# Kernel optimization log

Measured on AMD Instinct MI355X. Metric: run time of the kernel, lower is better.

Reference implementation:

```python
import jax, jax.numpy as jnp
import numpy as np

B, D, H, L = 65536, 512, 1024, 64
LOG2PI = float(np.log(2.0 * np.pi))


def setup_inputs() -> dict:
    key = jax.random.key(0)
    ks = jax.random.split(key, 16)
    s = jnp.float32(0.02)

    def w(k, shape):
        return jax.random.normal(k, shape, dtype=jnp.float32) * s

    return {
        "x": jax.random.normal(ks[0], (B, D), dtype=jnp.float32),
        "eps": jax.random.normal(ks[1], (B, L), dtype=jnp.float32),
        # encoder params (Linear stored as [in, out] for x @ W + b)
        "W_enc_h": w(ks[2], (D, H)), "b_enc_h": jnp.zeros((H,), jnp.float32),
        "W_enc_mu": w(ks[3], (H, L)), "b_enc_mu": jnp.zeros((L,), jnp.float32),
        "W_enc_lv": w(ks[4], (H, L)), "b_enc_lv": jnp.zeros((L,), jnp.float32),
        # decoder params
        "W_dec_h": w(ks[5], (L, H)), "b_dec_h": jnp.zeros((H,), jnp.float32),
        "W_dec_mu": w(ks[6], (H, D)), "b_dec_mu": jnp.zeros((D,), jnp.float32),
        "W_dec_lv": w(ks[7], (H, D)), "b_dec_lv": jnp.zeros((D,), jnp.float32),
    }


def reference(x, eps, W_enc_h, b_enc_h, W_enc_mu, b_enc_mu, W_enc_lv, b_enc_lv,
              W_dec_h, b_dec_h, W_dec_mu, b_dec_mu, W_dec_lv, b_dec_lv):
    beta = jnp.float32(1.0)
    # encoder
    h = jnp.tanh(x @ W_enc_h + b_enc_h)                      # [B, H]
    mu_z = h @ W_enc_mu + b_enc_mu                           # [B, L]
    lv_z = h @ W_enc_lv + b_enc_lv                           # [B, L]
    # reparameterised sample
    z = mu_z + jnp.exp(0.5 * lv_z) * eps                     # [B, L]
    # decoder
    hd = jnp.tanh(z @ W_dec_h + b_dec_h)                     # [B, H]
    mu_x = jax.nn.softmax(hd @ W_dec_mu + b_dec_mu, axis=-1) # [B, D]
    lv_x = hd @ W_dec_lv + b_dec_lv                          # [B, D]
    # KL(q(z|x) || N(0, I))
    kl = -0.5 * jnp.sum(1.0 + lv_z - mu_z ** 2 - jnp.exp(lv_z), axis=-1)  # [B]
    # diagonal Gaussian log-likelihood (closed form of MultivariateNormal
    # with diag_embed(exp(ln_var)) covariance)
    ln_pxz = -0.5 * jnp.sum(lv_x + (x - mu_x) ** 2 * jnp.exp(-lv_x) + LOG2PI, axis=-1)  # [B]
    return jnp.mean(ln_pxz - beta * kl)
```

## Files before the change

kernel.cpp:

```cpp
#include <hip/hip_runtime.h>

typedef unsigned char u8;
typedef unsigned short u16;
typedef unsigned int u32;
typedef long i64;
typedef __attribute__((ext_vector_type(2))) long long2v;
typedef __attribute__((ext_vector_type(4))) float floatx4;

#define LOG2PI_F 1.8378770664093453f

__device__ __forceinline__ u16 f2bf(float f) {
  union { float f; u32 i; } c; c.f = f;
  u32 i = c.i;
  u32 r = (i + 0x7fffu + ((i >> 16) & 1u)) >> 16;
  return (u16)r;
}
__device__ __forceinline__ float bf2f(u16 u) {
  union { u32 i; float f; } c; c.i = ((u32)u) << 16; return c.f;
}
__device__ __forceinline__ u8 f2fp8(float f) {
  int p = __builtin_amdgcn_cvt_pk_fp8_f32(f, f, 0, false);
  return (u8)(p & 0xff);
}
__device__ __forceinline__ u32 pk4fp8(float a, float b, float c, float d) {
  int lo = __builtin_amdgcn_cvt_pk_fp8_f32(a, b, 0, false);
  int v  = __builtin_amdgcn_cvt_pk_fp8_f32(c, d, lo, true);
  return (u32)v;
}
__device__ __forceinline__ void llds16(const void* g, void* l) {
  __builtin_amdgcn_global_load_lds(
      (const __attribute__((address_space(1))) u32*)g,
      (__attribute__((address_space(3))) u32*)l, 16, 0, 0);
}
__device__ __forceinline__ u32 permk(u32 k) {
  u32 g = k & ~63u, o = (k >> 3) & 7u, r = k & 7u;
  u32 po = ((o & 3u) << 1) | (o >> 2);
  return g | (po << 3) | r;
}

#define INV_4096  2.44140625e-4f
#define INV_16384 6.103515625e-5f

__global__ void pack_xb(const float* __restrict__ in, u32* __restrict__ out, int n4) {
  int i = blockIdx.x * 256 + threadIdx.x;
  if (i >= n4) return;
  const float4 v = ((const float4*)in)[i];
  int row = i >> 7;
  int k = (i & 127) << 2;
  int kp = permk(k);
  out[(row << 7) + (kp >> 2)] = pk4fp8(v.x * 16.f, v.y * 16.f, v.z * 16.f, v.w * 16.f);
}

__global__ void pack_wt(const float* __restrict__ W, u8* __restrict__ Wt, int K, int N) {
  int idx = blockIdx.x * 256 + threadIdx.x;
  if (idx >= K * N) return;
  int k = idx / N, n = idx - k * N;
  Wt[(size_t)n * K + permk(k)] = f2fp8(W[idx] * 256.f);
}

__global__ void pack_wt2(const float* __restrict__ W1, const float* __restrict__ W2,
                         u8* __restrict__ Wt, int K, int N1, int N2) {
  int idx = blockIdx.x * 256 + threadIdx.x;
  if (idx >= (N1 + N2) * K) return;
  int n = idx / K, k = idx - n * K;
  float v = (n < N1) ? W1[(size_t)k * N1 + n] : W2[(size_t)k * N2 + (n - N1)];
  Wt[(size_t)n * K + permk(k)] = f2fp8(v * 256.f);
}

__global__ void catf(const float* __restrict__ a, const float* __restrict__ b,
                     float* __restrict__ o, int n1, int n2) {
  int i = blockIdx.x * 256 + threadIdx.x;
  if (i < n1) o[i] = a[i];
  else if (i < n1 + n2) o[i] = b[i - n1];
}

template <int EPI>
__global__ __launch_bounds__(256) void gemm_bt(
    const u8* __restrict__ A, const u8* __restrict__ Bt,
    const float* __restrict__ bias, void* __restrict__ Cv,
    float inv, float outs, int M, int N, int K) {
  __shared__ __align__(16) u8 As[128 * 64];
  __shared__ __align__(16) u8 Bs[128 * 64];
  const int t = threadIdx.x;
  const int wave = t >> 6, lane = t & 63;
  const int quad = lane >> 4, l16 = lane & 15;
  const int bm = blockIdx.y * 128, bn = blockIdx.x * 128;
  const int wm = (wave >> 1) * 64, wn = (wave & 1) * 64;

  floatx4 acc[4][4];
#pragma unroll
  for (int i = 0; i < 4; ++i)
#pragma unroll
    for (int j = 0; j < 4; ++j) acc[i][j] = (floatx4){0.f, 0.f, 0.f, 0.f};

  for (int kt = 0; kt < K; kt += 64) {
#pragma unroll
    for (int i = 0; i < 2; ++i) {
      int c = i * 256 + t;
      int r = c >> 2, kcS = c & 3;
      int kc = kcS ^ ((r >> 1) & 3);
      llds16(A + (size_t)(bm + r) * K + kt + kc * 16, &As[c * 16]);
      llds16(Bt + (size_t)(bn + r) * K + kt + kc * 16, &Bs[c * 16]);
    }
    __builtin_amdgcn_s_waitcnt(0);
    __syncthreads();

    long2v a2[4], b2[4];
#pragma unroll
    for (int mi = 0; mi < 4; ++mi) {
      int m = wm + mi * 16 + l16;
      a2[mi] = *(const long2v*)&As[(4 * m + (quad ^ ((m >> 1) & 3))) * 16];
    }
#pragma unroll
    for (int ni = 0; ni < 4; ++ni) {
      int n = wn + ni * 16 + l16;
      b2[ni] = *(const long2v*)&Bs[(4 * n + (quad ^ ((n >> 1) & 3))) * 16];
    }
#pragma unroll
    for (int h = 0; h < 2; ++h)
#pragma unroll
      for (int mi = 0; mi < 4; ++mi)
#pragma unroll
        for (int ni = 0; ni < 4; ++ni)
          acc[mi][ni] = __builtin_amdgcn_mfma_f32_16x16x32_fp8_fp8(
              a2[mi][h], b2[ni][h], acc[mi][ni], 0, 0, 0);
    __syncthreads();
  }

#pragma unroll
  for (int ni = 0; ni < 4; ++ni) {
    int col = bn + wn + ni * 16 + l16;
    float bv = bias[col];
#pragma unroll
    for (int mi = 0; mi < 4; ++mi) {
#pragma unroll
      for (int r = 0; r < 4; ++r) {
        int row = bm + wm + mi * 16 + quad * 4 + r;
        float v = acc[mi][ni][r] * inv + bv;
        if (EPI == 0) {
          ((u8*)Cv)[(size_t)row * N + permk(col)] = f2fp8(tanhf(v) * outs);
        } else {
          ((u16*)Cv)[(size_t)row * N + col] = f2bf(v);
        }
      }
    }
  }
}

__global__ __launch_bounds__(256) void gemm_z(
    const u8* __restrict__ A, const u8* __restrict__ Bt,
    const float* __restrict__ bias, const float* __restrict__ eps,
    u8* __restrict__ z, float* __restrict__ accp, int M, int K) {
  __shared__ __align__(16) u8 As[128 * 64];
  __shared__ __align__(16) u8 Bs[128 * 64];
  __shared__ float sexp[128 * 64];
  const int t = threadIdx.x;
  const int wave = t >> 6, lane = t & 63;
  const int quad = lane >> 4, l16 = lane & 15;
  const int bm = blockIdx.y * 128;
  const int wm = (wave >> 1) * 64, wn = (wave & 1) * 64;

  floatx4 acc[4][4];
#pragma unroll
  for (int i = 0; i < 4; ++i)
#pragma unroll
    for (int j = 0; j < 4; ++j) acc[i][j] = (floatx4){0.f, 0.f, 0.f, 0.f};

  for (int kt = 0; kt < K; kt += 64) {
#pragma unroll
    for (int i = 0; i < 2; ++i) {
      int c = i * 256 + t;
      int r = c >> 2, kcS = c & 3;
      int kc = kcS ^ ((r >> 1) & 3);
      llds16(A + (size_t)(bm + r) * K + kt + kc * 16, &As[c * 16]);
      llds16(Bt + (size_t)r * K + kt + kc * 16, &Bs[c * 16]);
    }
    __builtin_amdgcn_s_waitcnt(0);
    __syncthreads();

    long2v a2[4], b2[4];
#pragma unroll
    for (int mi = 0; mi < 4; ++mi) {
      int m = wm + mi * 16 + l16;
      a2[mi] = *(const long2v*)&As[(4 * m + (quad ^ ((m >> 1) & 3))) * 16];
    }
#pragma unroll
    for (int ni = 0; ni < 4; ++ni) {
      int n = wn + ni * 16 + l16;
      b2[ni] = *(const long2v*)&Bs[(4 * n + (quad ^ ((n >> 1) & 3))) * 16];
    }
#pragma unroll
    for (int h = 0; h < 2; ++h)
#pragma unroll
      for (int mi = 0; mi < 4; ++mi)
#pragma unroll
        for (int ni = 0; ni < 4; ++ni)
          acc[mi][ni] = __builtin_amdgcn_mfma_f32_16x16x32_fp8_fp8(
              a2[mi][h], b2[ni][h], acc[mi][ni], 0, 0, 0);
    __syncthreads();
  }

  const bool is_lv = (wave & 1);
  float kl = 0.f;
#pragma unroll
  for (int ni = 0; ni < 4; ++ni) {
    int col = wn + ni * 16 + l16;
    float bv = bias[col];
#pragma unroll
    for (int mi = 0; mi < 4; ++mi) {
#pragma unroll
      for (int r = 0; r < 4; ++r) {
        int row = wm + mi * 16 + quad * 4 + r;
        float v = acc[mi][ni][r] * INV_16384 + bv;
        if (is_lv) {
          kl += 1.0f + v - __expf(v);
          sexp[row * 64 + (col - 64)] = __expf(0.5f * v);
        } else {
          kl -= v * v;
        }
      }
    }
  }
  __syncthreads();
  if (!is_lv) {
#pragma unroll
    for (int ni = 0; ni < 4; ++ni) {
      int col = wn + ni * 16 + l16;
      float bv = bias[col];
#pragma unroll
      for (int mi = 0; mi < 4; ++mi) {
#pragma unroll
        for (int r = 0; r < 4; ++r) {
          int row = wm + mi * 16 + quad * 4 + r;
          float mu = acc[mi][ni][r] * INV_16384 + bv;
          size_t grow = (size_t)(bm + row);
          float ep = eps[grow * 64 + col];
          z[grow * 64 + permk(col)] = f2fp8((mu + sexp[row * 64 + col] * ep) * 16.f);
        }
      }
    }
  }
  kl *= 0.5f;
  for (int off = 32; off > 0; off >>= 1) kl += __shfl_xor(kl, off, 64);
  __shared__ float s4[4];
  if (lane == 0) s4[wave] = kl;
  __syncthreads();
  if (t == 0) atomicAdd(accp, s4[0] + s4[1] + s4[2] + s4[3]);
}

__global__ __launch_bounds__(256) void lik_kernel(
    const u16* __restrict__ loglv, const float* __restrict__ x,
    float* __restrict__ acc) {
  typedef __attribute__((ext_vector_type(8))) short short8;
  const int wave = threadIdx.x >> 6, lane = threadIdx.x & 63;
  float wacc = 0.f;
  for (int rr = 0; rr < 8; ++rr) {
    int row = blockIdx.x * 32 + wave * 8 + rr;
    const u16* Lr = loglv + (size_t)row * 1024;
    short8 lg8 = ((const short8*)Lr)[lane];
    float lg[8];
#pragma unroll
    for (int j = 0; j < 8; ++j) lg[j] = bf2f((u16)lg8[j]);
    float mx = lg[0];
#pragma unroll
    for (int j = 1; j < 8; ++j) mx = fmaxf(mx, lg[j]);
    for (int off = 32; off > 0; off >>= 1) mx = fmaxf(mx, __shfl_xor(mx, off, 64));
    float e[8], s = 0.f;
#pragma unroll
    for (int j = 0; j < 8; ++j) { e[j] = __expf(lg[j] - mx); s += e[j]; }
    for (int off = 32; off > 0; off >>= 1) s += __shfl_xor(s, off, 64);
    float inv_s = 1.0f / s;
    short8 lv8 = ((const short8*)Lr)[64 + lane];
    const float* xr = x + (size_t)row * 512 + lane * 8;
    float4 x0 = *(const float4*)xr, x1 = *(const float4*)(xr + 4);
    float xs[8] = {x0.x, x0.y, x0.z, x0.w, x1.x, x1.y, x1.z, x1.w};
    float T = 0.f;
#pragma unroll
    for (int j = 0; j < 8; ++j) {
      float lv = bf2f((u16)lv8[j]);
      float d = xs[j] - e[j] * inv_s;
      T += lv + d * d * __expf(-lv) + LOG2PI_F;
    }
    for (int off = 32; off > 0; off >>= 1) T += __shfl_xor(T, off, 64);
    if (lane == 0) wacc += -0.5f * T;
  }
  __shared__ float s4[4];
  if (lane == 0) s4[wave] = wacc;
  __syncthreads();
  if (threadIdx.x == 0) atomicAdd(acc, s4[0] + s4[1] + s4[2] + s4[3]);
}

__global__ void fin_kernel(const float* __restrict__ acc, float* __restrict__ out) {
  out[0] = acc[0] * (1.0f / 65536.0f);
}

extern "C" void kernel_launch(void* const* d_in, const int* in_sizes, int n_in,
                              void* d_out, int out_size, void* d_ws, size_t ws_size,
                              hipStream_t stream) {
  const int B = 65536, D = 512, H = 1024, L = 64;
  const float* x       = (const float*)d_in[0];
  const float* eps     = (const float*)d_in[1];
  const float* W_enc_h = (const float*)d_in[2];
  const float* b_enc_h = (const float*)d_in[3];
  const float* W_enc_mu= (const float*)d_in[4];
  const float* b_enc_mu= (const float*)d_in[5];
  const float* W_enc_lv= (const float*)d_in[6];
  const float* b_enc_lv= (const float*)d_in[7];
  const float* W_dec_h = (const float*)d_in[8];
  const float* b_dec_h = (const float*)d_in[9];
  const float* W_dec_mu= (const float*)d_in[10];
  const float* b_dec_mu= (const float*)d_in[11];
  const float* W_dec_lv= (const float*)d_in[12];
  const float* b_dec_lv= (const float*)d_in[13];

  char* ws = (char*)d_ws;
  u8*   Wt_eh  = (u8*)(ws + 0);
  u8*   Wt_z   = (u8*)(ws + 524288);
  u8*   Wt_dh  = (u8*)(ws + 655360);
  u8*   Wt_dx  = (u8*)(ws + 720896);
  float* bh    = (float*)(ws + 2097152);
  float* bz    = (float*)(ws + 2101248);
  float* bdh   = (float*)(ws + 2105344);
  float* bdx   = (float*)(ws + 2109440);
  float* acc   = (float*)(ws + 2113536);
  u8*   hbuf   = (u8*)(ws + 4194304);
  u8*   xb     = (u8*)(ws + 71303168);
  u8*   zbuf   = (u8*)(ws + 104857600);
  u16*  loglv  = (u16*)(ws + 109051904);

  hipMemsetAsync(acc, 0, 256, stream);

  pack_xb<<<(B * D / 4 + 255) / 256, 256, 0, stream>>>(x, (u32*)xb, B * D / 4);
  pack_wt<<<(D * H + 255) / 256, 256, 0, stream>>>(W_enc_h, Wt_eh, D, H);
  pack_wt2<<<(H * 2 * L + 255) / 256, 256, 0, stream>>>(W_enc_mu, W_enc_lv, Wt_z, H, L, L);
  pack_wt<<<(L * H + 255) / 256, 256, 0, stream>>>(W_dec_h, Wt_dh, L, H);
  pack_wt2<<<(H * 2 * D + 255) / 256, 256, 0, stream>>>(W_dec_mu, W_dec_lv, Wt_dx, H, D, D);
  catf<<<(H + 255) / 256, 256, 0, stream>>>(b_enc_h, b_enc_h, bh, H, 0);
  catf<<<(2 * L + 255) / 256, 256, 0, stream>>>(b_enc_mu, b_enc_lv, bz, L, L);
  catf<<<(H + 255) / 256, 256, 0, stream>>>(b_dec_h, b_dec_h, bdh, H, 0);
  catf<<<(2 * D + 255) / 256, 256, 0, stream>>>(b_dec_mu, b_dec_lv, bdx, D, D);

  gemm_bt<0><<<dim3(H / 128, B / 128), 256, 0, stream>>>(
      xb, Wt_eh, bh, hbuf, INV_4096, 64.f, B, H, D);
  gemm_z<<<dim3(1, B / 128), 256, 0, stream>>>(hbuf, Wt_z, bz, eps, zbuf, acc, B, H);
  gemm_bt<0><<<dim3(H / 128, B / 128), 256, 0, stream>>>(
      zbuf, Wt_dh, bdh, hbuf, INV_4096, 64.f, B, H, L);
  gemm_bt<2><<<dim3(1024 / 128, B / 128), 256, 0, stream>>>(
      hbuf, Wt_dx, bdx, loglv, INV_16384, 0.f, B, 1024, H);
  lik_kernel<<<B / 32, 256, 0, stream>>>(loglv, x, acc);
  fin_kernel<<<1, 1, 0, stream>>>(acc, (float*)d_out);
}
```

Measured before the change: 618.7 us.

## Add 256x256-tile FP8 GEMM with 4-stage LDS pipeline for large GEMMs

```diff
diff --git a/kernel.cpp b/kernel.cpp
--- a/kernel.cpp
+++ b/kernel.cpp
@@ -133,6 +133,108 @@
     float bv = bias[col];
 #pragma unroll
     for (int mi = 0; mi < 4; ++mi) {
+#pragma unroll
+      for (int r = 0; r < 4; ++r) {
+        int row = bm + wm + mi * 16 + quad * 4 + r;
+        float v = acc[mi][ni][r] * inv + bv;
+        if (EPI == 0) {
+          ((u8*)Cv)[(size_t)row * N + permk(col)] = f2fp8(tanhf(v) * outs);
+        } else {
+          ((u16*)Cv)[(size_t)row * N + col] = f2bf(v);
+        }
+      }
+    }
+  }
+}
+
+template <int EPI>
+__global__ __launch_bounds__(512, 2) void gemm256(
+    const u8* __restrict__ A, const u8* __restrict__ Bt,
+    const float* __restrict__ bias, void* __restrict__ Cv,
+    float inv, float outs, int M, int N, int K) {
+  __shared__ __align__(16) u8 lds[4][2][256 * 64];
+  const int t = threadIdx.x;
+  const int wave = t >> 6, lane = t & 63;
+  const int quad = lane >> 4, l16 = lane & 15;
+  const int nbx = N >> 8;
+  const int nwg = nbx * (M >> 8);
+  int raw = blockIdx.x + nbx * blockIdx.y;
+  int wgid = ((nwg & 7) == 0) ? ((raw & 7) * (nwg >> 3) + (raw >> 3)) : raw;
+  const int bm = (wgid / nbx) << 8, bn = (wgid % nbx) << 8;
+  const int wm = (wave >> 2) * 128, wn = (wave & 3) * 64;
+  const int nt = K >> 6;
+
+  auto stage = [&](int b, int kt) {
+#pragma unroll
+    for (int i = 0; i < 2; ++i) {
+      int c = i * 512 + t;
+      int r = c >> 2, kcS = c & 3;
+      int kc = kcS ^ ((r >> 1) & 3);
+      llds16(A + (size_t)(bm + r) * K + kt + kc * 16, &lds[b][0][c * 16]);
+    }
+#pragma unroll
+    for (int i = 0; i < 2; ++i) {
+      int c = i * 512 + t;
+      int r = c >> 2, kcS = c & 3;
+      int kc = kcS ^ ((r >> 1) & 3);
+      llds16(Bt + (size_t)(bn + r) * K + kt + kc * 16, &lds[b][1][c * 16]);
+    }
+  };
+
+  floatx4 acc[8][4];
+#pragma unroll
+  for (int i = 0; i < 8; ++i)
+#pragma unroll
+    for (int j = 0; j < 4; ++j) acc[i][j] = (floatx4){0.f, 0.f, 0.f, 0.f};
+
+  stage(0, 0);
+  if (nt > 1) stage(1, 64);
+  if (nt > 2) stage(2, 128);
+
+  for (int ti = 0; ti < nt; ++ti) {
+    const int b = ti & 3;
+    if (ti + 3 < nt) stage((ti + 3) & 3, (ti + 3) << 6);
+    int rem = nt - 1 - ti;
+    if (rem >= 3)      { asm volatile("s_waitcnt vmcnt(12)" ::: "memory"); }
+    else if (rem == 2) { asm volatile("s_waitcnt vmcnt(8)" ::: "memory"); }
+    else if (rem == 1) { asm volatile("s_waitcnt vmcnt(4)" ::: "memory"); }
+    else               { asm volatile("s_waitcnt vmcnt(0)" ::: "memory"); }
+    __builtin_amdgcn_s_barrier();
+
+    const u8* As = &lds[b][0][0];
+    const u8* Bs = &lds[b][1][0];
+    long2v a2[8], b2[4];
+#pragma unroll
+    for (int mi = 0; mi < 8; ++mi) {
+      int m = wm + mi * 16 + l16;
+      a2[mi] = *(const long2v*)&As[(4 * m + (quad ^ ((m >> 1) & 3))) * 16];
+    }
+#pragma unroll
+    for (int ni = 0; ni < 4; ++ni) {
+      int n = wn + ni * 16 + l16;
+      b2[ni] = *(const long2v*)&Bs[(4 * n + (quad ^ ((n >> 1) & 3))) * 16];
+    }
+    __builtin_amdgcn_s_setprio(1);
+#pragma unroll
+    for (int h = 0; h < 2; ++h)
+#pragma unroll
+      for (int mi = 0; mi < 8; ++mi)
+#pragma unroll
+        for (int ni = 0; ni < 4; ++ni)
+          acc[mi][ni] = __builtin_amdgcn_mfma_f32_16x16x32_fp8_fp8(
+              a2[mi][h], b2[ni][h], acc[mi][ni], 0, 0, 0);
+    __builtin_amdgcn_s_setprio(0);
+    asm volatile("s_waitcnt lgkmcnt(0)" ::: "memory");
+    __builtin_amdgcn_sched_barrier(0);
+    __builtin_amdgcn_s_barrier();
+  }
+
+#pragma unroll
+  for (int ni = 0; ni < 4; ++ni) {
+    int col = bn + wn + ni * 16 + l16;
+    float bv = bias[col];
+#pragma unroll
+    for (int mi = 0; mi < 8; ++mi) {
 #pragma unroll
       for (int r = 0; r < 4; ++r) {
         int row = bm + wm + mi * 16 + quad * 4 + r;
@@ -340,12 +442,12 @@
   catf<<<(H + 255) / 256, 256, 0, stream>>>(b_dec_h, b_dec_h, bdh, H, 0);
   catf<<<(2 * D + 255) / 256, 256, 0, stream>>>(b_dec_mu, b_dec_lv, bdx, D, D);
 
-  gemm_bt<0><<<dim3(H / 128, B / 128), 256, 0, stream>>>(
+  gemm256<0><<<dim3(H / 256, B / 256), 512, 0, stream>>>(
       xb, Wt_eh, bh, hbuf, INV_4096, 64.f, B, H, D);
   gemm_z<<<dim3(1, B / 128), 256, 0, stream>>>(hbuf, Wt_z, bz, eps, zbuf, acc, B, H);
   gemm_bt<0><<<dim3(H / 128, B / 128), 256, 0, stream>>>(
       zbuf, Wt_dh, bdh, hbuf, INV_4096, 64.f, B, H, L);
-  gemm_bt<2><<<dim3(1024 / 128, B / 128), 256, 0, stream>>>(
+  gemm256<2><<<dim3(1024 / 256, B / 256), 512, 0, stream>>>(
       hbuf, Wt_dx, bdx, loglv, INV_16384, 0.f, B, 1024, H);
   lik_kernel<<<B / 32, 256, 0, stream>>>(loglv, x, acc);
   fin_kernel<<<1, 1, 0, stream>>>(acc, (float*)d_out);
```

Measured after the change: 640.4 us. 1.03x slower.
